# Kernel tuning notes

Measured on AMD Instinct MI355X. Metric: run time of the kernel, lower is better.

The kernel has to match this reference:

```python
import jax, jax.numpy as jnp
import numpy as np

NEG = -1000000.0  # mask fill value used by the torch module

def setup_inputs() -> dict:
    key = jax.random.key(0)
    ks = jax.random.split(key, 7)
    B, Tq, Tk, Din, H, Dv = 16, 128, 256, 64, 256, 256
    return {
        "queries": jax.random.normal(ks[0], (B, Tq, Din), dtype=jnp.float32),
        "keys": jax.random.normal(ks[1], (B, Tk, Din), dtype=jnp.float32),
        "values": jax.random.normal(ks[2], (B, Tk, Dv), dtype=jnp.float32),
        "valid_lens": jax.random.randint(ks[3], (B,), 0, Tk, dtype=jnp.int32),
        "wq": jax.random.normal(ks[4], (Din, H), dtype=jnp.float32) * 0.05,
        "wk": jax.random.normal(ks[5], (Din, H), dtype=jnp.float32) * 0.05,
        "wv": jax.random.normal(ks[6], (H,), dtype=jnp.float32) * 0.05,
    }

def reference(queries, keys, values, valid_lens, wq, wk, wv):
    # Project queries and keys to num_hiddens
    q = jnp.einsum("bqd,dh->bqh", queries, wq)       # [B,Tq,H]
    k = jnp.einsum("bkd,dh->bkh", keys, wk)          # [B,Tk,H]
    # Additive features [B,Tq,Tk,H] -> tanh -> scalar score via wv
    feats = jnp.tanh(q[:, :, None, :] + k[:, None, :, :])
    scores = jnp.einsum("bqkh,h->bqk", feats, wv)    # [B,Tq,Tk]
    # Masked softmax over last axis; valid_lens [B] broadcasts over Tq
    Tk = scores.shape[-1]
    mask = jnp.arange(Tk)[None, None, :] < valid_lens[:, None, None]
    scores = jnp.where(mask, scores, NEG)
    attn = jax.nn.softmax(scores, axis=-1)           # [B,Tq,Tk]
    return jnp.einsum("bqk,bkv->bqv", attn, values)  # [B,Tq,Dv]
```

## Files before the change

kernel.cpp:

```cpp
#include <hip/hip_runtime.h>

#define B_  16
#define TQ  128
#define TK  256
#define DIN 64
#define H_  256
#define DV  256
#define HT  8
#define QT  4
#define NEG -1000000.0f

#define SCALE  2.8853900817779268f
#define LOG2E  1.4426950408889634f

__device__ inline float fast_exp2(float x) { return __builtin_amdgcn_exp2f(x); }
__device__ inline float fast_rcp(float x)  { return __builtin_amdgcn_rcpf(x); }

__global__ __launch_bounds__(256) void proj_k_kernel(
    const float* __restrict__ keys, const float* __restrict__ wk,
    float* __restrict__ kpT)
{
    int b  = blockIdx.x >> 5;
    int h0 = (blockIdx.x & 31) * HT;
    int t  = threadIdx.x;
    const float* krow = keys + (b * TK + t) * DIN;
    float acc[HT];
    #pragma unroll
    for (int hh = 0; hh < HT; ++hh) acc[hh] = 0.f;
    #pragma unroll 4
    for (int d = 0; d < DIN; ++d) {
        float kv = krow[d];
        #pragma unroll
        for (int hh = 0; hh < HT; ++hh)
            acc[hh] = fmaf(kv, wk[d * H_ + h0 + hh], acc[hh]);
    }
    #pragma unroll
    for (int hh = 0; hh < HT; ++hh)
        kpT[(b * H_ + h0 + hh) * TK + t] = acc[hh] * SCALE;
}

__device__ inline float waveMax(float v) {
    #pragma unroll
    for (int off = 32; off > 0; off >>= 1) v = fmaxf(v, __shfl_xor(v, off, 64));
    return v;
}
__device__ inline float waveSum(float v) {
    #pragma unroll
    for (int off = 32; off > 0; off >>= 1) v += __shfl_xor(v, off, 64);
    return v;
}

__global__ __launch_bounds__(512) void attn_kernel(
    const float* __restrict__ queries, const float* __restrict__ wq,
    const float* __restrict__ kpT,
    const float* __restrict__ values, const int* __restrict__ valid_lens,
    const float* __restrict__ wv, float* __restrict__ out)
{
    __shared__ float4 qs4[H_];
    __shared__ float  wvL[H_];
    __shared__ float  scoreP[2][QT][TK];
    __shared__ float4 attnT[TK];

    int bx   = blockIdx.x;
    int xcd  = bx & 7;
    int i    = bx >> 3;
    int b    = xcd + 8 * (i & 1);
    int q0   = (i >> 1) * QT;
    int t    = threadIdx.x;
    int half = t >> 8;
    int lo   = t & 255;

    if (t < 256) {
        const float* qbase = queries + (b * TQ + q0) * DIN;
        float a0 = 0.f, a1 = 0.f, a2 = 0.f, a3 = 0.f;
        #pragma unroll
        for (int d = 0; d < DIN; ++d) {
            float w = wq[d * H_ + t];
            a0 = fmaf(qbase[d],           w, a0);
            a1 = fmaf(qbase[DIN + d],     w, a1);
            a2 = fmaf(qbase[2 * DIN + d], w, a2);
            a3 = fmaf(qbase[3 * DIN + d], w, a3);
        }
        qs4[t] = make_float4(a0 * SCALE, a1 * SCALE, a2 * SCALE, a3 * SCALE);
        wvL[t] = wv[t];
    }
    __syncthreads();

    {
        const float* kcol = kpT + b * H_ * TK + lo;
        int h0 = half * (H_ / 2);
        float s0 = 0.f, s1 = 0.f, s2 = 0.f, s3 = 0.f;
        #pragma unroll 4
        for (int hh = 0; hh < H_ / 2; ++hh) {
            int h = h0 + hh;
            float  kv  = kcol[h * TK];
            float4 qv  = qs4[h];
            float  wvh = wvL[h];
            float u0 = qv.x + kv, u1 = qv.y + kv, u2 = qv.z + kv, u3 = qv.w + kv;
            float r0 = fast_rcp(fast_exp2(u0) + 1.f);
            float r1 = fast_rcp(fast_exp2(u1) + 1.f);
            float r2 = fast_rcp(fast_exp2(u2) + 1.f);
            float r3 = fast_rcp(fast_exp2(u3) + 1.f);
            s0 = fmaf(wvh, fmaf(-2.f, r0, 1.f), s0);
            s1 = fmaf(wvh, fmaf(-2.f, r1, 1.f), s1);
            s2 = fmaf(wvh, fmaf(-2.f, r2, 1.f), s2);
            s3 = fmaf(wvh, fmaf(-2.f, r3, 1.f), s3);
        }
        scoreP[half][0][lo] = s0;
        scoreP[half][1][lo] = s1;
        scoreP[half][2][lo] = s2;
        scoreP[half][3][lo] = s3;
    }
    __syncthreads();

    if (t < 256) {
        int w    = t >> 6;
        int lane = t & 63;
        int vl   = valid_lens[b];
        float v0 = scoreP[0][w][lane      ] + scoreP[1][w][lane      ];
        float v1 = scoreP[0][w][lane +  64] + scoreP[1][w][lane +  64];
        float v2 = scoreP[0][w][lane + 128] + scoreP[1][w][lane + 128];
        float v3 = scoreP[0][w][lane + 192] + scoreP[1][w][lane + 192];
        v0 = (lane       < vl) ? v0 : NEG;
        v1 = (lane +  64 < vl) ? v1 : NEG;
        v2 = (lane + 128 < vl) ? v2 : NEG;
        v3 = (lane + 192 < vl) ? v3 : NEG;
        float m  = waveMax(fmaxf(fmaxf(v0, v1), fmaxf(v2, v3)));
        float p0 = fast_exp2((v0 - m) * LOG2E);
        float p1 = fast_exp2((v1 - m) * LOG2E);
        float p2 = fast_exp2((v2 - m) * LOG2E);
        float p3 = fast_exp2((v3 - m) * LOG2E);
        float dr = fast_rcp(waveSum(p0 + p1 + p2 + p3));
        ((float*)&attnT[lane      ])[w] = p0 * dr;
        ((float*)&attnT[lane +  64])[w] = p1 * dr;
        ((float*)&attnT[lane + 128])[w] = p2 * dr;
        ((float*)&attnT[lane + 192])[w] = p3 * dr;
    }
    __syncthreads();

    {
        const float* vcol = values + b * TK * DV + lo;
        int k0 = half * (TK / 2);
        float o0 = 0.f, o1 = 0.f, o2 = 0.f, o3 = 0.f;
        #pragma unroll 8
        for (int kk = 0; kk < TK / 2; ++kk) {
            int k = k0 + kk;
            float  vv = vcol[k * DV];
            float4 a  = attnT[k];
            o0 = fmaf(a.x, vv, o0);
            o1 = fmaf(a.y, vv, o1);
            o2 = fmaf(a.z, vv, o2);
            o3 = fmaf(a.w, vv, o3);
        }
        if (half == 1) {
            scoreP[1][0][lo] = o0;
            scoreP[1][1][lo] = o1;
            scoreP[1][2][lo] = o2;
            scoreP[1][3][lo] = o3;
        }
        __syncthreads();
        if (half == 0) {
            float* orow = out + (b * TQ + q0) * DV + lo;
            orow[0]      = o0 + scoreP[1][0][lo];
            orow[DV]     = o1 + scoreP[1][1][lo];
            orow[2 * DV] = o2 + scoreP[1][2][lo];
            orow[3 * DV] = o3 + scoreP[1][3][lo];
        }
    }
}

extern "C" void kernel_launch(void* const* d_in, const int* in_sizes, int n_in,
                              void* d_out, int out_size, void* d_ws, size_t ws_size,
                              hipStream_t stream) {
    const float* queries    = (const float*)d_in[0];
    const float* keys       = (const float*)d_in[1];
    const float* values     = (const float*)d_in[2];
    const int*   valid_lens = (const int*)  d_in[3];
    const float* wq         = (const float*)d_in[4];
    const float* wk         = (const float*)d_in[5];
    const float* wv         = (const float*)d_in[6];
    float* out = (float*)d_out;

    float* kpT = (float*)d_ws;

    proj_k_kernel<<<B_ * (H_ / HT), 256, 0, stream>>>(keys, wk, kpT);
    attn_kernel<<<B_ * (TQ / QT), 512, 0, stream>>>(queries, wq, kpT, values,
                                                    valid_lens, wv, out);
}
```

Before: 116.0 us.

## Skip masked key columns in projection, scoring and PV; halve queries per block

The key projection, the tanh score loop and the attention-times-values loop now skip key positions beyond valid_len. Scores are skipped in 64-wide groups, and when valid_len is zero the PV loop still runs over all keys. This removes transcendental and memory work that the mask would zero out anyway. Queries per block drop from 4 to 2, doubling the grid, and wv is packed into the same shared float4 as the projected queries. In exchange, per-block work becomes data-dependent, which can cause load imbalance across batches, and each block repeats the query projection setup for fewer rows.

```diff
diff --git a/kernel.cpp b/kernel.cpp
--- a/kernel.cpp
+++ b/kernel.cpp
@@ -7,7 +7,7 @@
 #define H_  256
 #define DV  256
 #define HT  8
-#define QT  4
+#define QT  2
 #define NEG -1000000.0f
 
 #define SCALE  2.8853900817779268f
@@ -18,11 +18,13 @@
 
 __global__ __launch_bounds__(256) void proj_k_kernel(
     const float* __restrict__ keys, const float* __restrict__ wk,
-    float* __restrict__ kpT)
+    float* __restrict__ kpT, const int* __restrict__ valid_lens)
 {
     int b  = blockIdx.x >> 5;
     int h0 = (blockIdx.x & 31) * HT;
     int t  = threadIdx.x;
+    int vlC = (valid_lens[b] + 63) & ~63;
+    if (t >= vlC) return;
     const float* krow = keys + (b * TK + t) * DIN;
     float acc[HT];
     #pragma unroll
@@ -56,10 +58,9 @@
     const float* __restrict__ values, const int* __restrict__ valid_lens,
     const float* __restrict__ wv, float* __restrict__ out)
 {
-    __shared__ float4 qs4[H_];
-    __shared__ float  wvL[H_];
+    __shared__ float4 qw4[H_];
     __shared__ float  scoreP[2][QT][TK];
-    __shared__ float4 attnT[TK];
+    __shared__ float2 attnT[TK];
 
     int bx   = blockIdx.x;
     int xcd  = bx & 7;
@@ -69,54 +70,44 @@
     int t    = threadIdx.x;
     int half = t >> 8;
     int lo   = t & 255;
+    int vl   = valid_lens[b];
 
     if (t < 256) {
         const float* qbase = queries + (b * TQ + q0) * DIN;
-        float a0 = 0.f, a1 = 0.f, a2 = 0.f, a3 = 0.f;
+        float a0 = 0.f, a1 = 0.f;
         #pragma unroll
         for (int d = 0; d < DIN; ++d) {
             float w = wq[d * H_ + t];
-            a0 = fmaf(qbase[d],           w, a0);
-            a1 = fmaf(qbase[DIN + d],     w, a1);
-            a2 = fmaf(qbase[2 * DIN + d], w, a2);
-            a3 = fmaf(qbase[3 * DIN + d], w, a3);
+            a0 = fmaf(qbase[d],       w, a0);
+            a1 = fmaf(qbase[DIN + d], w, a1);
         }
-        qs4[t] = make_float4(a0 * SCALE, a1 * SCALE, a2 * SCALE, a3 * SCALE);
-        wvL[t] = wv[t];
+        qw4[t] = make_float4(a0 * SCALE, a1 * SCALE, wv[t], 0.f);
     }
     __syncthreads();
 
-    {
+    if ((lo & 192) < vl) {
         const float* kcol = kpT + b * H_ * TK + lo;
         int h0 = half * (H_ / 2);
-        float s0 = 0.f, s1 = 0.f, s2 = 0.f, s3 = 0.f;
+        float s0 = 0.f, s1 = 0.f;
         #pragma unroll 4
         for (int hh = 0; hh < H_ / 2; ++hh) {
             int h = h0 + hh;
-            float  kv  = kcol[h * TK];
-            float4 qv  = qs4[h];
-            float  wvh = wvL[h];
-            float u0 = qv.x + kv, u1 = qv.y + kv, u2 = qv.z + kv, u3 = qv.w + kv;
+            float  kv = kcol[h * TK];
+            float4 qv = qw4[h];
+            float u0 = qv.x + kv, u1 = qv.y + kv;
             float r0 = fast_rcp(fast_exp2(u0) + 1.f);
             float r1 = fast_rcp(fast_exp2(u1) + 1.f);
-            float r2 = fast_rcp(fast_exp2(u2) + 1.f);
-            float r3 = fast_rcp(fast_exp2(u3) + 1.f);
-            s0 = fmaf(wvh, fmaf(-2.f, r0, 1.f), s0);
-            s1 = fmaf(wvh, fmaf(-2.f, r1, 1.f), s1);
-            s2 = fmaf(wvh, fmaf(-2.f, r2, 1.f), s2);
-            s3 = fmaf(wvh, fmaf(-2.f, r3, 1.f), s3);
+            s0 = fmaf(qv.z, fmaf(-2.f, r0, 1.f), s0);
+            s1 = fmaf(qv.z, fmaf(-2.f, r1, 1.f), s1);
         }
         scoreP[half][0][lo] = s0;
         scoreP[half][1][lo] = s1;
-        scoreP[half][2][lo] = s2;
-        scoreP[half][3][lo] = s3;
     }
     __syncthreads();
 
-    if (t < 256) {
+    if (t < 64 * QT) {
         int w    = t >> 6;
         int lane = t & 63;
-        int vl   = valid_lens[b];
         float v0 = scoreP[0][w][lane      ] + scoreP[1][w][lane      ];
         float v1 = scoreP[0][w][lane +  64] + scoreP[1][w][lane +  64];
         float v2 = scoreP[0][w][lane + 128] + scoreP[1][w][lane + 128];
@@ -139,32 +130,27 @@
     __syncthreads();
 
     {
+        int kLim = (vl == 0) ? TK : vl;
+        int k0   = half * (TK / 2);
+        int kEnd = min(k0 + TK / 2, kLim);
         const float* vcol = values + b * TK * DV + lo;
-        int k0 = half * (TK / 2);
-        float o0 = 0.f, o1 = 0.f, o2 = 0.f, o3 = 0.f;
-        #pragma unroll 8
-        for (int kk = 0; kk < TK / 2; ++kk) {
-            int k = k0 + kk;
+        float o0 = 0.f, o1 = 0.f;
+        #pragma unroll 4
+        for (int k = k0; k < kEnd; ++k) {
             float  vv = vcol[k * DV];
-            float4 a  = attnT[k];
+            float2 a  = attnT[k];
             o0 = fmaf(a.x, vv, o0);
             o1 = fmaf(a.y, vv, o1);
-            o2 = fmaf(a.z, vv, o2);
-            o3 = fmaf(a.w, vv, o3);
         }
         if (half == 1) {
             scoreP[1][0][lo] = o0;
             scoreP[1][1][lo] = o1;
-            scoreP[1][2][lo] = o2;
-            scoreP[1][3][lo] = o3;
         }
         __syncthreads();
         if (half == 0) {
             float* orow = out + (b * TQ + q0) * DV + lo;
-            orow[0]      = o0 + scoreP[1][0][lo];
-            orow[DV]     = o1 + scoreP[1][1][lo];
-            orow[2 * DV] = o2 + scoreP[1][2][lo];
-            orow[3 * DV] = o3 + scoreP[1][3][lo];
+            orow[0]  = o0 + scoreP[1][0][lo];
+            orow[DV] = o1 + scoreP[1][1][lo];
         }
     }
 }
@@ -183,7 +169,7 @@
 
     float* kpT = (float*)d_ws;
 
-    proj_k_kernel<<<B_ * (H_ / HT), 256, 0, stream>>>(keys, wk, kpT);
+    proj_k_kernel<<<B_ * (H_ / HT), 256, 0, stream>>>(keys, wk, kpT, valid_lens);
     attn_kernel<<<B_ * (TQ / QT), 512, 0, stream>>>(queries, wq, kpT, values,
                                                     valid_lens, wv, out);
 }
```

Result: no change. 115.3 us (-0.5%).
